# Kernel tuning notes

Hardware: AMD Instinct MI355X
Metric: run time of the kernel (lower is better)

## Reference

```python
import jax, jax.numpy as jnp
import numpy as np

NEG_BIG = -9e15
ALPHA = 0.2  # leaky relu slope


def setup_inputs() -> dict:
    key = jax.random.key(0)
    k_h, k_adj, k_W, k_a = jax.random.split(key, 4)
    N, F_in, F_out = 8192, 512, 64
    h = jax.random.normal(k_h, (N, F_in), dtype=jnp.float32)
    adj = jax.random.randint(k_adj, (N, N), 0, 2, dtype=jnp.int32)
    adj = adj.at[jnp.arange(N), jnp.arange(N)].set(1)  # self-loops (add_self_loops)
    # xavier_uniform with gain=1.414
    limW = 1.414 * np.sqrt(6.0 / (F_in + F_out))
    W = jax.random.uniform(k_W, (F_in, F_out), jnp.float32, -limW, limW)
    lima = 1.414 * np.sqrt(6.0 / (2 * F_out + 1))
    a = jax.random.uniform(k_a, (2 * F_out, 1), jnp.float32, -lima, lima)
    return {"h": h, "adj": adj, "W": W, "a": a}


def reference(h, adj, W, a):
    F_out = W.shape[1]
    Wh = h @ W                                  # [N, F_out]
    # a_input[i,j] = concat(Wh[i], Wh[j]); a_input @ a == Wh@a1 + (Wh@a2)^T
    a1, a2 = a[:F_out, 0], a[F_out:, 0]
    src = Wh @ a1                               # [N]
    dst = Wh @ a2                               # [N]
    e = jax.nn.leaky_relu(src[:, None] + dst[None, :], ALPHA)  # [N, N]
    att = jnp.where(adj > 0, e, NEG_BIG)
    att = jax.nn.softmax(att, axis=1)
    # dropout is identity in eval mode (training=False)
    return att @ Wh                             # [N, F_out]
```

## Files before the change

### kernel.cpp

```cpp
#include <hip/hip_runtime.h>
#include <hip/hip_bf16.h>

#define N 8192
#define FIN 512
#define FOUT 64
#define L2E 1.44269504089f
#define SPLIT 8
#define NTILES ((N / SPLIT) / 64)

typedef __attribute__((address_space(1))) const void* gas_cptr;
typedef __attribute__((address_space(3))) void* las_ptr;
typedef float f32x4 __attribute__((ext_vector_type(4)));
typedef short bf16x8 __attribute__((ext_vector_type(8)));

#if __has_builtin(__builtin_amdgcn_exp2f)
#define EXP2(x) __builtin_amdgcn_exp2f(x)
#else
#define EXP2(x) exp2f(x)
#endif

static __device__ __forceinline__ unsigned short f2bf_rne(float f) {
  unsigned u = __float_as_uint(f);
  u += 0x7FFFu + ((u >> 16) & 1u);
  return (unsigned short)(u >> 16);
}
static __device__ __forceinline__ unsigned fkey(float f) {
  unsigned u = __float_as_uint(f);
  return (u & 0x80000000u) ? ~u : (u | 0x80000000u);
}

__global__ __launch_bounds__(256) void k_wh(
    const float* __restrict__ h, const float* __restrict__ W,
    const float* __restrict__ a, unsigned short* __restrict__ WhT,
    float* __restrict__ src2, float* __restrict__ dst2,
    unsigned* __restrict__ dmaxk) {
  __shared__ __attribute__((aligned(16))) char wts[64 * 512 * 2];
  __shared__ __attribute__((aligned(16))) char hsb[2][64 * 64 * 2];

  const int t = threadIdx.x;
  const int w = t >> 6;
  const int ll = t & 63;
  const int lc = ll & 15;
  const int row0 = blockIdx.x * 64;

  {
    const int k0 = t * 2;
#pragma unroll
    for (int f4 = 0; f4 < 16; ++f4) {
      float4 x0 = *reinterpret_cast<const float4*>(&W[(size_t)k0 * FOUT + f4 * 4]);
      float4 x1 = *reinterpret_cast<const float4*>(&W[(size_t)(k0 + 1) * FOUT + f4 * 4]);
      const float e0[4] = {x0.x, x0.y, x0.z, x0.w};
      const float e1[4] = {x1.x, x1.y, x1.z, x1.w};
#pragma unroll
      for (int e = 0; e < 4; ++e) {
        int f = f4 * 4 + e;
        int bb = f * 1024 + k0 * 2;
        bb ^= (f & 7) << 4;
        *reinterpret_cast<ushort2*>(wts + bb) =
            make_ushort2(f2bf_rne(e0[e]), f2bf_rne(e1[e]));
      }
    }
  }
  __syncthreads();

  f32x4 acc[4];
#pragma unroll
  for (int c = 0; c < 4; ++c) acc[c] = (f32x4){0.f, 0.f, 0.f, 0.f};

  const int hrow = 16 * w + (ll >> 2);
  const float* hbase = &h[(size_t)(row0 + hrow) * FIN + (ll & 3) * 16];

#define LOADH(dst, kc)                                                        \
  do {                                                                        \
    dst[0] = *reinterpret_cast<const float4*>(hbase + (kc));                  \
    dst[1] = *reinterpret_cast<const float4*>(hbase + (kc) + 4);              \
    dst[2] = *reinterpret_cast<const float4*>(hbase + (kc) + 8);              \
    dst[3] = *reinterpret_cast<const float4*>(hbase + (kc) + 12);             \
  } while (0)

#define WRITEH(buf, src)                                                      \
  do {                                                                        \
    int bb0 = hrow * 128 + (ll & 3) * 32;                                     \
    bb0 ^= (hrow & 7) << 4;                                                   \
    _Pragma("unroll") for (int q = 0; q < 4; ++q) {                           \
      ushort4 u = make_ushort4(f2bf_rne(src[q].x), f2bf_rne(src[q].y),        \
                               f2bf_rne(src[q].z), f2bf_rne(src[q].w));       \
      *reinterpret_cast<ushort4*>(hsb[buf] + (bb0 ^ (q * 8))) = u;            \
    }                                                                         \
  } while (0)

#define MFMA_CHUNK(buf, kcb)                                                  \
  do {                                                                        \
    _Pragma("unroll") for (int k0 = 0; k0 < 2; ++k0) {                        \
      int arow = 16 * w + lc;                                                 \
      int ab = arow * 128 + k0 * 64 + ((ll >> 4) << 4);                       \
      ab ^= (arow & 7) << 4;                                                  \
      bf16x8 af = *reinterpret_cast<const bf16x8*>(hsb[buf] + ab);            \
      _Pragma("unroll") for (int c = 0; c < 4; ++c) {                         \
        int f = c * 16 + lc;                                                  \
        int bb = f * 1024 + (kcb) + k0 * 64 + ((ll >> 4) << 4);               \
        bb ^= (f & 7) << 4;                                                   \
        bf16x8 bfr = *reinterpret_cast<const bf16x8*>(wts + bb);              \
        acc[c] = __builtin_amdgcn_mfma_f32_16x16x32_bf16(af, bfr, acc[c], 0, 0, 0); \
      }                                                                       \
    }                                                                         \
  } while (0)

  float4 ha[4], hb[4];
  LOADH(ha, 0);
#pragma unroll
  for (int c2 = 0; c2 < 4; ++c2) {
    WRITEH(0, ha);
    LOADH(hb, (2 * c2 + 1) * 64);
    MFMA_CHUNK(0, (2 * c2) * 128);
    WRITEH(1, hb);
    if (c2 < 3) LOADH(ha, (2 * c2 + 2) * 64);
    MFMA_CHUNK(1, (2 * c2 + 1) * 128);
  }

  float a1v[4], a2v[4];
#pragma unroll
  for (int c = 0; c < 4; ++c) {
    a1v[c] = a[c * 16 + lc];
    a2v[c] = a[FOUT + c * 16 + lc];
  }
  float p1[4], p2[4];
#pragma unroll
  for (int q = 0; q < 4; ++q) {
    p1[q] = acc[0][q] * a1v[0] + acc[1][q] * a1v[1] + acc[2][q] * a1v[2] + acc[3][q] * a1v[3];
    p2[q] = acc[0][q] * a2v[0] + acc[1][q] * a2v[1] + acc[2][q] * a2v[2] + acc[3][q] * a2v[3];
  }
#pragma unroll
  for (int msk = 8; msk >= 1; msk >>= 1)
#pragma unroll
    for (int q = 0; q < 4; ++q) {
      p1[q] += __shfl_xor(p1[q], msk);
      p2[q] += __shfl_xor(p2[q], msk);
    }
#pragma unroll
  for (int q = 0; q < 4; ++q) { p1[q] *= L2E; p2[q] *= L2E; }

  const int r0 = row0 + 16 * w + ((ll >> 4) << 2);
  if (lc == 0) {
#pragma unroll
    for (int q = 0; q < 4; ++q) { src2[r0 + q] = p1[q]; dst2[r0 + q] = p2[q]; }
  }
#pragma unroll
  for (int c = 0; c < 4; ++c) {
    ushort4 u = make_ushort4(f2bf_rne(acc[c][0]), f2bf_rne(acc[c][1]),
                             f2bf_rne(acc[c][2]), f2bf_rne(acc[c][3]));
    *reinterpret_cast<ushort4*>(&WhT[(size_t)(c * 16 + lc) * N + r0]) = u;
  }
  float wm = fmaxf(fmaxf(p2[0], p2[1]), fmaxf(p2[2], p2[3]));
  wm = fmaxf(wm, __shfl_xor(wm, 16));
  wm = fmaxf(wm, __shfl_xor(wm, 32));
  if (ll == 0) atomicMax(dmaxk, fkey(wm));
#undef LOADH
#undef WRITEH
#undef MFMA_CHUNK
}

__global__ __launch_bounds__(256) void k_attn(
    const int* __restrict__ adj, const unsigned short* __restrict__ WhT,
    const float* __restrict__ src2, const float* __restrict__ dst2,
    const unsigned* __restrict__ dmaxk, float* __restrict__ out,
    float* __restrict__ Opart, float* __restrict__ lpart) {
  __shared__ __attribute__((aligned(16))) char pbs[8192];

  const int t = threadIdx.x;
  const int w = t >> 6;
  const int ll = t & 63;
  const int rg = t >> 4;
  const int cg = t & 15;
  const int i0 = rg * 4;
  const int lc = ll & 15;
  const int g16 = (ll >> 4) << 4;
  const int g8 = (ll >> 4) << 3;
  const int row0 = blockIdx.x * 64;
  const int jbase = blockIdx.y * (N / SPLIT);

  unsigned kk = dmaxk[0];
  const float dmax2 = (kk & 0x80000000u) ? __uint_as_float(kk & 0x7FFFFFFFu)
                                         : __uint_as_float(~kk);

  float s2v[4], m2[4], l[4];
#pragma unroll
  for (int r = 0; r < 4; ++r) {
    s2v[r] = src2[row0 + i0 + r];
    float x = s2v[r] + dmax2;
    m2[r] = fmaxf(x, 0.2f * x);
    l[r] = 0.f;
  }

  f32x4 acc[4];
#pragma unroll
  for (int c = 0; c < 4; ++c) acc[c] = (f32x4){0.f, 0.f, 0.f, 0.f};

  const int bsh = 0;
  (void)bsh;

  const int* ar0 = adj + (size_t)(row0 + i0 + 0) * N + jbase + cg * 4;
  const int* ar1 = adj + (size_t)(row0 + i0 + 1) * N + jbase + cg * 4;
  const int* ar2 = adj + (size_t)(row0 + i0 + 2) * N + jbase + cg * 4;
  const int* ar3 = adj + (size_t)(row0 + i0 + 3) * N + jbase + cg * 4;
  const float* dp = dst2 + jbase + cg * 4;

  int4 aS[4][4];
  float4 dS[4];

#define LOADT(s, jt_)                                                         \
  do {                                                                        \
    const int o_ = (jt_) * 64;                                                \
    aS[s][0] = *reinterpret_cast<const int4*>(ar0 + o_);                      \
    aS[s][1] = *reinterpret_cast<const int4*>(ar1 + o_);                      \
    aS[s][2] = *reinterpret_cast<const int4*>(ar2 + o_);                      \
    aS[s][3] = *reinterpret_cast<const int4*>(ar3 + o_);                      \
    dS[s] = *reinterpret_cast<const float4*>(dp + o_);                        \
  } while (0)

#pragma unroll
  for (int s = 0; s < 4; ++s) LOADT(s, s);

  const int arow = 16 * w + lc;
  int abz = (arow << 7);
  abz ^= (arow & 7) << 4;

  for (int jt4 = 0; jt4 < NTILES / 4; ++jt4) {
#pragma unroll
    for (int i = 0; i < 4; ++i) {
      const int jt = jt4 * 4 + i;
      const int j0 = jbase + jt * 64;

      bf16x8 bfr[2][4];
#pragma unroll
      for (int k0 = 0; k0 < 2; ++k0)
#pragma unroll
        for (int c = 0; c < 4; ++c)
          bfr[k0][c] = *reinterpret_cast<const bf16x8*>(
              &WhT[(size_t)(c * 16 + lc) * N + j0 + k0 * 32 + g8]);

      float p[4][4];
#pragma unroll
      for (int r = 0; r < 4; ++r) {
        const int aw[4] = {aS[i][r].x, aS[i][r].y, aS[i][r].z, aS[i][r].w};
        const float dvv[4] = {dS[i].x, dS[i].y, dS[i].z, dS[i].w};
#pragma unroll
        for (int jj = 0; jj < 4; ++jj) {
          float x = s2v[r] + dvv[jj];
          float e2 = fmaxf(x, 0.2f * x);
          float pe = EXP2(e2 - m2[r]);
          pe = aw[jj] > 0 ? pe : 0.f;
          p[r][jj] = pe;
          l[r] += pe;
        }
      }

      if (jt4 < NTILES / 4 - 1) LOADT(i, jt + 4);

#pragma unroll
      for (int r = 0; r < 4; ++r) {
        unsigned u0 = __float_as_uint(p[r][0]);
        unsigned u1 = __float_as_uint(p[r][1]);
        unsigned u2 = __float_as_uint(p[r][2]);
        unsigned u3 = __float_as_uint(p[r][3]);
        uint2 pk = make_uint2((u0 >> 16) | (u1 & 0xFFFF0000u),
                              (u2 >> 16) | (u3 & 0xFFFF0000u));
        int row = i0 + r;
        int ba = (row << 7) + (cg << 3);
        ba ^= (row & 7) << 4;
        *reinterpret_cast<uint2*>(pbs + ba) = pk;
      }

#pragma unroll
      for (int k0 = 0; k0 < 2; ++k0) {
        bf16x8 af = *reinterpret_cast<const bf16x8*>(pbs + (abz ^ (k0 * 64)) + k0 * 64 + g16 - (abz & 0) );
        af = *reinterpret_cast<const bf16x8*>(pbs + ((abz + k0 * 64 + g16) ^ 0));
        {
          int ab = (arow << 7) + k0 * 64 + g16;
          ab ^= (arow & 7) << 4;
          af = *reinterpret_cast<const bf16x8*>(pbs + ab);
        }
#pragma unroll
        for (int c = 0; c < 4; ++c)
          acc[c] = __builtin_amdgcn_mfma_f32_16x16x32_bf16(af, bfr[k0][c],
                                                           acc[c], 0, 0, 0);
      }
    }
  }
#undef LOADT

#pragma unroll
  for (int msk = 8; msk >= 1; msk >>= 1)
#pragma unroll
    for (int r = 0; r < 4; ++r) l[r] += __shfl_xor(l[r], msk);

  const int orow = row0 + 16 * w + ((ll >> 4) << 2);
  const int ocol = ll & 15;
  const int pb = blockIdx.y;
#pragma unroll
  for (int c = 0; c < 4; ++c)
#pragma unroll
    for (int q = 0; q < 4; ++q)
      Opart[((size_t)pb * N + orow + q) * FOUT + c * 16 + ocol] = acc[c][q];
  if (cg == 0) {
#pragma unroll
    for (int r = 0; r < 4; ++r)
      lpart[(size_t)pb * N + row0 + i0 + r] = l[r];
  }
}

__global__ __launch_bounds__(256) void k_combine(
    const float* __restrict__ Opart, const float* __restrict__ lpart,
    float* __restrict__ out) {
  int idx = blockIdx.x * 256 + threadIdx.x;
  int row = idx >> 6;
  float num = 0.f, den = 0.f;
#pragma unroll
  for (int k = 0; k < SPLIT; ++k) {
    num += Opart[(size_t)k * N * FOUT + idx];
    den += lpart[(size_t)k * N + row];
  }
  out[idx] = num / den;
}

extern "C" void kernel_launch(void* const* d_in, const int* in_sizes, int n_in,
                              void* d_out, int out_size, void* d_ws, size_t ws_size,
                              hipStream_t stream) {
  const float* h = (const float*)d_in[0];
  const int* adj = (const int*)d_in[1];
  const float* W = (const float*)d_in[2];
  const float* a = (const float*)d_in[3];
  float* out = (float*)d_out;

  unsigned short* WhT = (unsigned short*)d_ws;
  float* src2 = (float*)(WhT + (size_t)FOUT * N);
  float* dst2 = src2 + N;
  unsigned* dmaxk = (unsigned*)(dst2 + N);
  float* Opart = (float*)(dmaxk + 64);
  float* lpart = Opart + (size_t)SPLIT * N * FOUT;

  hipMemsetAsync(dmaxk, 0, 4, stream);
  k_wh<<<dim3(N / 64), 256, 0, stream>>>(h, W, a, WhT, src2, dst2, dmaxk);
  k_attn<<<dim3(N / 64, SPLIT), 256, 0, stream>>>(adj, WhT, src2, dst2, dmaxk,
                                                  out, Opart, lpart);
  k_combine<<<dim3((N * FOUT) / 256), 256, 0, stream>>>(Opart, lpart, out);
}
```

Baseline: 126.0 us.

## Double split-K, cut prefetch depth to two, add occupancy launch bound

Raises the column split of the attention kernel from 8 to 16, so the grid has twice as many blocks. The split is now chosen at runtime and halved until the partial buffers fit the workspace. The adjacency prefetch ring drops from four tiles to two, and __launch_bounds__(256,4) is added to cut register pressure and raise occupancy on this memory-bound adjacency stream. In exchange, the combine kernel reads twice as many partial outputs, and the shallower prefetch may expose more load latency.

New measurement: 233.4 us. 1.85x slower.

```diff
diff --git a/kernel.cpp b/kernel.cpp
--- a/kernel.cpp
+++ b/kernel.cpp
@@ -5,8 +5,7 @@
 #define FIN 512
 #define FOUT 64
 #define L2E 1.44269504089f
-#define SPLIT 8
-#define NTILES ((N / SPLIT) / 64)
+#define SPLIT 16
 
 typedef __attribute__((address_space(1))) const void* gas_cptr;
 typedef __attribute__((address_space(3))) void* las_ptr;
@@ -160,11 +159,11 @@
 #undef MFMA_CHUNK
 }
 
-__global__ __launch_bounds__(256) void k_attn(
+__global__ __launch_bounds__(256, 4) void k_attn(
     const int* __restrict__ adj, const unsigned short* __restrict__ WhT,
     const float* __restrict__ src2, const float* __restrict__ dst2,
     const unsigned* __restrict__ dmaxk, float* __restrict__ out,
-    float* __restrict__ Opart, float* __restrict__ lpart) {
+    float* __restrict__ Opart, float* __restrict__ lpart, const int split) {
   __shared__ __attribute__((aligned(16))) char pbs[8192];
 
   const int t = threadIdx.x;
@@ -177,7 +176,8 @@
   const int g16 = (ll >> 4) << 4;
   const int g8 = (ll >> 4) << 3;
   const int row0 = blockIdx.x * 64;
-  const int jbase = blockIdx.y * (N / SPLIT);
+  const int jbase = blockIdx.y * (N / split);
+  const int ntiles = (N / split) / 64;
 
   unsigned kk = dmaxk[0];
   const float dmax2 = (kk & 0x80000000u) ? __uint_as_float(kk & 0x7FFFFFFFu)
@@ -196,98 +196,91 @@
 #pragma unroll
   for (int c = 0; c < 4; ++c) acc[c] = (f32x4){0.f, 0.f, 0.f, 0.f};
 
-  const int bsh = 0;
-  (void)bsh;
-
   const int* ar0 = adj + (size_t)(row0 + i0 + 0) * N + jbase + cg * 4;
   const int* ar1 = adj + (size_t)(row0 + i0 + 1) * N + jbase + cg * 4;
   const int* ar2 = adj + (size_t)(row0 + i0 + 2) * N + jbase + cg * 4;
   const int* ar3 = adj + (size_t)(row0 + i0 + 3) * N + jbase + cg * 4;
   const float* dp = dst2 + jbase + cg * 4;
 
-  int4 aS[4][4];
-  float4 dS[4];
-
-#define LOADT(s, jt_)                                                         \
+  int4 a0[4], a1[4];
+  float4 d0, d1;
+
+#define LOADT0(jt_)                                                           \
   do {                                                                        \
     const int o_ = (jt_) * 64;                                                \
-    aS[s][0] = *reinterpret_cast<const int4*>(ar0 + o_);                      \
-    aS[s][1] = *reinterpret_cast<const int4*>(ar1 + o_);                      \
-    aS[s][2] = *reinterpret_cast<const int4*>(ar2 + o_);                      \
-    aS[s][3] = *reinterpret_cast<const int4*>(ar3 + o_);                      \
-    dS[s] = *reinterpret_cast<const float4*>(dp + o_);                        \
-  } while (0)
-
-#pragma unroll
-  for (int s = 0; s < 4; ++s) LOADT(s, s);
+    a0[0] = *reinterpret_cast<const int4*>(ar0 + o_);                         \
+    a0[1] = *reinterpret_cast<const int4*>(ar1 + o_);                         \
+    a0[2] = *reinterpret_cast<const int4*>(ar2 + o_);                         \
+    a0[3] = *reinterpret_cast<const int4*>(ar3 + o_);                         \
+    d0 = *reinterpret_cast<const float4*>(dp + o_);                           \
+  } while (0)
+#define LOADT1(jt_)                                                           \
+  do {                                                                        \
+    const int o_ = (jt_) * 64;                                                \
+    a1[0] = *reinterpret_cast<const int4*>(ar0 + o_);                         \
+    a1[1] = *reinterpret_cast<const int4*>(ar1 + o_);                         \
+    a1[2] = *reinterpret_cast<const int4*>(ar2 + o_);                         \
+    a1[3] = *reinterpret_cast<const int4*>(ar3 + o_);                         \
+    d1 = *reinterpret_cast<const float4*>(dp + o_);                           \
+  } while (0)
 
   const int arow = 16 * w + lc;
-  int abz = (arow << 7);
-  abz ^= (arow & 7) << 4;
-
-  for (int jt4 = 0; jt4 < NTILES / 4; ++jt4) {
-#pragma unroll
-    for (int i = 0; i < 4; ++i) {
-      const int jt = jt4 * 4 + i;
-      const int j0 = jbase + jt * 64;
-
-      bf16x8 bfr[2][4];
-#pragma unroll
-      for (int k0 = 0; k0 < 2; ++k0)
-#pragma unroll
-        for (int c = 0; c < 4; ++c)
-          bfr[k0][c] = *reinterpret_cast<const bf16x8*>(
-              &WhT[(size_t)(c * 16 + lc) * N + j0 + k0 * 32 + g8]);
-
-      float p[4][4];
-#pragma unroll
-      for (int r = 0; r < 4; ++r) {
-        const int aw[4] = {aS[i][r].x, aS[i][r].y, aS[i][r].z, aS[i][r].w};
-        const float dvv[4] = {dS[i].x, dS[i].y, dS[i].z, dS[i].w};
-#pragma unroll
-        for (int jj = 0; jj < 4; ++jj) {
-          float x = s2v[r] + dvv[jj];
-          float e2 = fmaxf(x, 0.2f * x);
-          float pe = EXP2(e2 - m2[r]);
-          pe = aw[jj] > 0 ? pe : 0.f;
-          p[r][jj] = pe;
-          l[r] += pe;
-        }
-      }
-
-      if (jt4 < NTILES / 4 - 1) LOADT(i, jt + 4);
-
-#pragma unroll
-      for (int r = 0; r < 4; ++r) {
-        unsigned u0 = __float_as_uint(p[r][0]);
-        unsigned u1 = __float_as_uint(p[r][1]);
-        unsigned u2 = __float_as_uint(p[r][2]);
-        unsigned u3 = __float_as_uint(p[r][3]);
-        uint2 pk = make_uint2((u0 >> 16) | (u1 & 0xFFFF0000u),
-                              (u2 >> 16) | (u3 & 0xFFFF0000u));
-        int row = i0 + r;
-        int ba = (row << 7) + (cg << 3);
-        ba ^= (row & 7) << 4;
-        *reinterpret_cast<uint2*>(pbs + ba) = pk;
-      }
-
-#pragma unroll
-      for (int k0 = 0; k0 < 2; ++k0) {
-        bf16x8 af = *reinterpret_cast<const bf16x8*>(pbs + (abz ^ (k0 * 64)) + k0 * 64 + g16 - (abz & 0) );
-        af = *reinterpret_cast<const bf16x8*>(pbs + ((abz + k0 * 64 + g16) ^ 0));
-        {
-          int ab = (arow << 7) + k0 * 64 + g16;
-          ab ^= (arow & 7) << 4;
-          af = *reinterpret_cast<const bf16x8*>(pbs + ab);
-        }
-#pragma unroll
-        for (int c = 0; c < 4; ++c)
-          acc[c] = __builtin_amdgcn_mfma_f32_16x16x32_bf16(af, bfr[k0][c],
-                                                           acc[c], 0, 0, 0);
-      }
-    }
-  }
-#undef LOADT
+
+#define TILE_BODY(AB, DB, LOADM, jt_)                                         \
+  {                                                                           \
+    const int j0 = jbase + (jt_) * 64;                                        \
+    bf16x8 bfr[2][4];                                                         \
+    _Pragma("unroll") for (int k0 = 0; k0 < 2; ++k0)                          \
+      _Pragma("unroll") for (int c = 0; c < 4; ++c)                           \
+        bfr[k0][c] = *reinterpret_cast<const bf16x8*>(                        \
+            &WhT[(size_t)(c * 16 + lc) * N + j0 + k0 * 32 + g8]);             \
+    float p[4][4];                                                            \
+    _Pragma("unroll") for (int r = 0; r < 4; ++r) {                           \
+      const int aw[4] = {AB[r].x, AB[r].y, AB[r].z, AB[r].w};                 \
+      const float dvv[4] = {DB.x, DB.y, DB.z, DB.w};                          \
+      _Pragma("unroll") for (int jj = 0; jj < 4; ++jj) {                      \
+        float x = s2v[r] + dvv[jj];                                           \
+        float e2 = fmaxf(x, 0.2f * x);                                        \
+        float pe = EXP2(e2 - m2[r]);                                          \
+        pe = aw[jj] > 0 ? pe : 0.f;                                           \
+        p[r][jj] = pe;                                                        \
+        l[r] += pe;                                                           \
+      }                                                                       \
+    }                                                                         \
+    if ((jt_) + 2 < ntiles) LOADM((jt_) + 2);                                 \
+    _Pragma("unroll") for (int r = 0; r < 4; ++r) {                           \
+      unsigned u0 = __float_as_uint(p[r][0]);                                 \
+      unsigned u1 = __float_as_uint(p[r][1]);                                 \
+      unsigned u2 = __float_as_uint(p[r][2]);                                 \
+      unsigned u3 = __float_as_uint(p[r][3]);                                 \
+      uint2 pk = make_uint2((u0 >> 16) | (u1 & 0xFFFF0000u),                  \
+                            (u2 >> 16) | (u3 & 0xFFFF0000u));                 \
+      int row = i0 + r;                                                       \
+      int ba = (row << 7) + (cg << 3);                                        \
+      ba ^= (row & 7) << 4;                                                   \
+      *reinterpret_cast<uint2*>(pbs + ba) = pk;                               \
+    }                                                                         \
+    _Pragma("unroll") for (int k0 = 0; k0 < 2; ++k0) {                        \
+      int ab = (arow << 7) + k0 * 64 + g16;                                   \
+      ab ^= (arow & 7) << 4;                                                  \
+      bf16x8 af = *reinterpret_cast<const bf16x8*>(pbs + ab);                 \
+      _Pragma("unroll") for (int c = 0; c < 4; ++c)                           \
+        acc[c] = __builtin_amdgcn_mfma_f32_16x16x32_bf16(af, bfr[k0][c],      \
+                                                         acc[c], 0, 0, 0);    \
+    }                                                                         \
+  }
+
+  LOADT0(0);
+  LOADT1(1);
+
+#pragma unroll 1
+  for (int jt = 0; jt < ntiles; jt += 2) {
+    TILE_BODY(a0, d0, LOADT0, jt);
+    TILE_BODY(a1, d1, LOADT1, jt + 1);
+  }
+#undef TILE_BODY
+#undef LOADT0
+#undef LOADT1
 
 #pragma unroll
   for (int msk = 8; msk >= 1; msk >>= 1)
@@ -307,16 +300,16 @@
     for (int r = 0; r < 4; ++r)
       lpart[(size_t)pb * N + row0 + i0 + r] = l[r];
   }
+  (void)out;
 }
 
 __global__ __launch_bounds__(256) void k_combine(
     const float* __restrict__ Opart, const float* __restrict__ lpart,
-    float* __restrict__ out) {
+    float* __restrict__ out, const int split) {
   int idx = blockIdx.x * 256 + threadIdx.x;
   int row = idx >> 6;
   float num = 0.f, den = 0.f;
-#pragma unroll
-  for (int k = 0; k < SPLIT; ++k) {
+  for (int k = 0; k < split; ++k) {
     num += Opart[(size_t)k * N * FOUT + idx];
     den += lpart[(size_t)k * N + row];
   }
@@ -337,11 +330,17 @@
   float* dst2 = src2 + N;
   unsigned* dmaxk = (unsigned*)(dst2 + N);
   float* Opart = (float*)(dmaxk + 64);
-  float* lpart = Opart + (size_t)SPLIT * N * FOUT;
+
+  const size_t base_bytes = (size_t)FOUT * N * 2 + 2 * N * 4 + 256;
+  int split = SPLIT;
+  while (split > 1 &&
+         base_bytes + (size_t)split * ((size_t)N * FOUT + N) * 4 > ws_size)
+    split >>= 1;
+  float* lpart = Opart + (size_t)split * N * FOUT;
 
   hipMemsetAsync(dmaxk, 0, 4, stream);
   k_wh<<<dim3(N / 64), 256, 0, stream>>>(h, W, a, WhT, src2, dst2, dmaxk);
-  k_attn<<<dim3(N / 64, SPLIT), 256, 0, stream>>>(adj, WhT, src2, dst2, dmaxk,
-                                                  out, Opart, lpart);
-  k_combine<<<dim3((N * FOUT) / 256), 256, 0, stream>>>(Opart, lpart, out);
-}
+  k_attn<<<dim3(N / 64, split), 256, 0, stream>>>(adj, WhT, src2, dst2, dmaxk,
+                                                  out, Opart, lpart, split);
+  k_combine<<<dim3((N * FOUT) / 256), 256, 0, stream>>>(Opart, lpart, out, split);
+}
```
